# Kernel optimization log

Hardware: AMD Instinct MI355X
Metric: run time of the kernel (lower is better)

Reference implementation:

```python
import jax, jax.numpy as jnp
import numpy as np

N_NODES = 50000
N_EDGES = 800000
IN_FEAT = 128
HIDDEN = 128
N_CLASSES = 32


def setup_inputs() -> dict:
    key = jax.random.key(0)
    ks = jax.random.split(key, 8)
    x = jax.random.normal(ks[0], (N_NODES, IN_FEAT), dtype=jnp.float32)
    edge_index = jax.random.randint(ks[1], (2, N_EDGES), 0, N_NODES, dtype=jnp.int64)
    def glorot(k, fan_in, fan_out):
        s = jnp.sqrt(2.0 / (fan_in + fan_out)).astype(jnp.float32)
        return jax.random.normal(k, (fan_in, fan_out), dtype=jnp.float32) * s
    W1 = glorot(ks[2], IN_FEAT, 2 * HIDDEN)
    b1 = jnp.zeros((2 * HIDDEN,), dtype=jnp.float32)
    W2 = glorot(ks[3], 2 * HIDDEN, HIDDEN)
    b2 = jnp.zeros((HIDDEN,), dtype=jnp.float32)
    W3 = glorot(ks[4], HIDDEN, N_CLASSES)
    b3 = jnp.zeros((N_CLASSES,), dtype=jnp.float32)
    return {"x": x, "edge_index": edge_index, "W1": W1, "b1": b1,
            "W2": W2, "b2": b2, "W3": W3, "b3": b3}


def _gcn_norm(edge_index, num_nodes):
    # PyG GCNConv default: add self-loops, symmetric normalization D^-1/2 (A+I) D^-1/2
    loops = jnp.arange(num_nodes, dtype=edge_index.dtype)
    src = jnp.concatenate([edge_index[0], loops])
    dst = jnp.concatenate([edge_index[1], loops])
    ones = jnp.ones_like(dst, dtype=jnp.float32)
    deg = jax.ops.segment_sum(ones, dst, num_segments=num_nodes)
    dinv = jnp.where(deg > 0, 1.0 / jnp.sqrt(deg), 0.0)
    norm = dinv[src] * dinv[dst]  # [E + N]
    return src, dst, norm


def _gcn_conv(x, src, dst, norm, W, b, num_nodes):
    h = x @ W                               # [N, out]
    msg = h[src] * norm[:, None]            # gather + per-edge scale, [E+N, out]
    agg = jax.ops.segment_sum(msg, dst, num_segments=num_nodes)  # scatter-add
    return agg + b


def reference(x, edge_index, W1, b1, W2, b2, W3, b3):
    n = x.shape[0]
    src, dst, norm = _gcn_norm(edge_index, n)
    h = jax.nn.relu(_gcn_conv(x, src, dst, norm, W1, b1, n))
    h = jax.nn.relu(_gcn_conv(h, src, dst, norm, W2, b2, n))
    return _gcn_conv(h, src, dst, norm, W3, b3, n)
```

## Files before the change

### kernel.cpp

```cpp
#include <hip/hip_runtime.h>
#include <hip/hip_fp16.h>

#define NN 50000
#define NE 800000
#define NBKT 391
#define P1B 256

typedef __attribute__((ext_vector_type(8))) _Float16 half8v;
typedef __attribute__((ext_vector_type(4))) float f32x4;

static inline size_t align_up(size_t x, size_t a) { return (x + a - 1) & ~(a - 1); }

union U8 {
    ushort4 u;
    __half2 h[2];
};

__device__ __forceinline__ float4 u8_to_f4(ushort4 uu) {
    U8 c;
    c.u = uu;
    float2 f01 = __half22float2(c.h[0]);
    float2 f23 = __half22float2(c.h[1]);
    return make_float4(f01.x, f01.y, f23.x, f23.y);
}

__device__ __forceinline__ ushort4 f4_to_u8(float4 v) {
    U8 c;
    c.h[0] = __floats2half2_rn(v.x, v.y);
    c.h[1] = __floats2half2_rn(v.z, v.w);
    return c.u;
}

__device__ __forceinline__ void gload_lds16(const unsigned short* g, unsigned short* l) {
    __builtin_amdgcn_global_load_lds(
        (const __attribute__((address_space(1))) unsigned int*)g,
        (__attribute__((address_space(3))) unsigned int*)l,
        16, 0, 0);
}

__device__ __forceinline__ int detect64(const int* __restrict__ e) {
    int ok = 1;
    for (int k = 1; k < 64; k += 2) ok &= (e[k] == 0);
    return ok;
}

__global__ __launch_bounds__(256) void bucket_hist(const int* __restrict__ e,
                                                   int* __restrict__ base,
                                                   const float* __restrict__ W1,
                                                   const float* __restrict__ W2,
                                                   const float* __restrict__ W3,
                                                   unsigned short* __restrict__ w1t,
                                                   unsigned short* __restrict__ w2t,
                                                   unsigned short* __restrict__ w3t,
                                                   int E) {
    __shared__ int hist[NBKT];
    const int is64 = detect64(e);
    for (int t = threadIdx.x; t < NBKT; t += 256) hist[t] = 0;
    __syncthreads();
    const int chunk = (E + P1B - 1) / P1B;
    const int b0 = blockIdx.x * chunk;
    const int b1 = min(E, b0 + chunk);
    for (int i = b0 + threadIdx.x; i < b1; i += 256) {
        int d = is64 ? e[2 * (E + i)] : e[E + i];
        atomicAdd(&hist[d >> 7], 1);
    }
    for (int i = blockIdx.x * 256 + threadIdx.x; i < 69632; i += P1B * 256) {
        const float* W;
        unsigned short* th;
        int K, M, j;
        if (i < 32768)      { W = W1; th = w1t; K = 128; M = 256; j = i; }
        else if (i < 65536) { W = W2; th = w2t; K = 256; M = 128; j = i - 32768; }
        else                { W = W3; th = w3t; K = 128; M = 32;  j = i - 65536; }
        int k = j / M, m = j % M;
        th[(size_t)m * K + k] = __half_as_ushort(__float2half_rn(W[j]));
    }
    __syncthreads();
    for (int t = threadIdx.x; t < NBKT; t += 256)
        base[blockIdx.x * NBKT + t] = hist[t];
}

__global__ __launch_bounds__(512) void colsum_scan(int* __restrict__ base,
                                                   int* __restrict__ bstart) {
    __shared__ int s[512];
    const int t = threadIdx.x;
    int total = 0;
    if (t < NBKT) {
        for (int b0 = 0; b0 < P1B; b0 += 8) {
            int v[8];
#pragma unroll
            for (int u = 0; u < 8; ++u) v[u] = base[(size_t)(b0 + u) * NBKT + t];
#pragma unroll
            for (int u = 0; u < 8; ++u) {
                int nv = v[u];
                base[(size_t)(b0 + u) * NBKT + t] = total;
                total += nv;
            }
        }
    }
    s[t] = (t < NBKT) ? total : 0;
    __syncthreads();
    for (int off = 1; off < 512; off <<= 1) {
        int tv = (t >= off) ? s[t - off] : 0;
        __syncthreads();
        s[t] += tv;
        __syncthreads();
    }
    if (t < NBKT) bstart[t] = s[t] - total;
    if (t == 0) bstart[NBKT] = s[511];
}

__global__ __launch_bounds__(256) void bucket_scatter(const int* __restrict__ e,
                                                      const int* __restrict__ bstart,
                                                      const int* __restrict__ base,
                                                      unsigned* __restrict__ pairs, int E) {
    __shared__ int cur[NBKT];
    const int is64 = detect64(e);
    for (int t = threadIdx.x; t < NBKT; t += 256)
        cur[t] = bstart[t] + base[blockIdx.x * NBKT + t];
    __syncthreads();
    const int chunk = (E + P1B - 1) / P1B;
    const int b0 = blockIdx.x * chunk;
    const int b1 = min(E, b0 + chunk);
    for (int i = b0 + threadIdx.x; i < b1; i += 256) {
        int s = is64 ? e[2 * i] : e[i];
        int d = is64 ? e[2 * (E + i)] : e[E + i];
        int pos = atomicAdd(&cur[d >> 7], 1);
        pairs[pos] = (unsigned)s | ((unsigned)(d & 127) << 16);
    }
}

__global__ __launch_bounds__(256) void bucket_finalize(const unsigned* __restrict__ pairs,
                                                       const int* __restrict__ bstart,
                                                       const float* __restrict__ x,
                                                       int2* __restrict__ ninfo,
                                                       float* __restrict__ dinv,
                                                       unsigned short* __restrict__ csr,
                                                       unsigned short* __restrict__ xh, int n) {
    __shared__ int ldeg[128];
    __shared__ int lscan[128];
    __shared__ int cur[128];
    __shared__ float sdinv[128];
    const int bkt = blockIdx.x;
    const int s0 = bstart[bkt], s1 = bstart[bkt + 1];
    if (threadIdx.x < 128) ldeg[threadIdx.x] = 0;
    __syncthreads();
    for (int i = s0 + threadIdx.x; i < s1; i += 256)
        atomicAdd(&ldeg[pairs[i] >> 16], 1);
    __syncthreads();
    if (threadIdx.x < 128) lscan[threadIdx.x] = ldeg[threadIdx.x];
    __syncthreads();
    for (int off = 1; off < 128; off <<= 1) {
        int v = 0;
        if (threadIdx.x < 128 && threadIdx.x >= off) v = lscan[threadIdx.x - off];
        __syncthreads();
        if (threadIdx.x < 128) lscan[threadIdx.x] += v;
        __syncthreads();
    }
    if (threadIdx.x < 128) {
        int node = (bkt << 7) + threadIdx.x;
        int exc = s0 + lscan[threadIdx.x] - ldeg[threadIdx.x];
        cur[threadIdx.x] = exc;
        float di = rsqrtf((float)(ldeg[threadIdx.x] + 1));
        sdinv[threadIdx.x] = di;
        if (node < n) {
            ninfo[node] = make_int2(exc, ldeg[threadIdx.x]);
            dinv[node] = di;
        }
    }
    __syncthreads();
    for (int i = s0 + threadIdx.x; i < s1; i += 256) {
        unsigned pr = pairs[i];
        int pos = atomicAdd(&cur[pr >> 16], 1);
        csr[pos] = (unsigned short)(pr & 0xFFFFu);
    }
    for (int idx = threadIdx.x; idx < 128 * 32; idx += 256) {
        int ln = idx >> 5;
        int c4 = idx & 31;
        int node = (bkt << 7) + ln;
        if (node < n) {
            float4 v = ((const float4*)x)[(size_t)node * 32 + c4];
            float s = sdinv[ln];
            v.x *= s; v.y *= s; v.z *= s; v.w *= s;
            ((ushort4*)xh)[(size_t)node * 32 + c4] = f4_to_u8(v);
        }
    }
}

__global__ __launch_bounds__(256) void gemm12(
    const unsigned short* __restrict__ A,
    const unsigned short* __restrict__ W1t,
    const unsigned short* __restrict__ W2t,
    const float* __restrict__ b1,
    const float* __restrict__ dinv,
    unsigned short* __restrict__ H2,
    int N) {
    __shared__ unsigned short sA[128][128];
    __shared__ unsigned short sW[128][128];
    __shared__ unsigned short sH[128][136];

    const int tid = threadIdx.x;
    const int lane = tid & 63;
    const int w = tid >> 6;
    const int wr = w >> 1, wc = w & 1;
    const int row0 = blockIdx.x * 128;
    const int rsel = lane & 15;
    const int cq = lane >> 4;

#pragma unroll
    for (int b = 0; b < 2048; b += 256) {
        int idx = b + tid;
        int r = idx >> 4, s = idx & 15;
        int gr = row0 + r;
        int sp = (s & 8) | ((s ^ r) & 7);
        if (gr < N) gload_lds16(&A[(size_t)gr * 128 + sp * 8], &sA[0][0] + idx * 8);
    }

    f32x4 acc2[4][4];
#pragma unroll
    for (int m = 0; m < 4; ++m)
#pragma unroll
        for (int nn = 0; nn < 4; ++nn) {
            f32x4 z = {0.f, 0.f, 0.f, 0.f};
            acc2[m][nn] = z;
        }

    for (int half = 0; half < 2; ++half) {
        __syncthreads();
#pragma unroll
        for (int b = 0; b < 2048; b += 256) {
            int idx = b + tid;
            int r = idx >> 4, s = idx & 15;
            int sp = (s & 8) | ((s ^ r) & 7);
            gload_lds16(&W1t[(size_t)(half * 128 + r) * 128 + sp * 8], &sW[0][0] + idx * 8);
        }
        __syncthreads();

        f32x4 acc1[4][4];
#pragma unroll
        for (int m = 0; m < 4; ++m)
#pragma unroll
            for (int nn = 0; nn < 4; ++nn) {
                f32x4 z = {0.f, 0.f, 0.f, 0.f};
                acc1[m][nn] = z;
            }
#pragma unroll
        for (int ks = 0; ks < 4; ++ks) {
            half8v af[4], wf[4];
            int c = ks * 4 + cq;
#pragma unroll
            for (int m = 0; m < 4; ++m) {
                int rr = wr * 64 + m * 16 + rsel;
                int cp = (c & 8) | ((c ^ rr) & 7);
                af[m] = *(const half8v*)&sA[rr][cp * 8];
            }
#pragma unroll
            for (int nn = 0; nn < 4; ++nn) {
                int rr = wc * 64 + nn * 16 + rsel;
                int cp = (c & 8) | ((c ^ rr) & 7);
                wf[nn] = *(const half8v*)&sW[rr][cp * 8];
            }
#pragma unroll
            for (int m = 0; m < 4; ++m)
#pragma unroll
                for (int nn = 0; nn < 4; ++nn)
                    acc1[m][nn] = __builtin_amdgcn_mfma_f32_16x16x32_f16(af[m], wf[nn], acc1[m][nn], 0, 0, 0);
        }

        float b1v[4];
#pragma unroll
        for (int nn = 0; nn < 4; ++nn)
            b1v[nn] = b1[half * 128 + wc * 64 + nn * 16 + rsel];
#pragma unroll
        for (int m = 0; m < 4; ++m)
#pragma unroll
            for (int nn = 0; nn < 4; ++nn)
#pragma unroll
                for (int r = 0; r < 4; ++r) {
                    int rl = wr * 64 + m * 16 + cq * 4 + r;
                    int cl = wc * 64 + nn * 16 + rsel;
                    float v = fmaxf(acc1[m][nn][r] + b1v[nn], 0.f);
                    sH[rl][cl] = __half_as_ushort(__float2half_rn(v));
                }
        __syncthreads();

#pragma unroll
        for (int b = 0; b < 2048; b += 256) {
            int idx = b + tid;
            int r = idx >> 4, s = idx & 15;
            int sp = (s & 8) | ((s ^ r) & 7);
            gload_lds16(&W2t[(size_t)r * 256 + half * 128 + sp * 8], &sW[0][0] + idx * 8);
        }
        __syncthreads();

#pragma unroll
        for (int ks = 0; ks < 4; ++ks) {
            half8v ah[4], wf[4];
            int koff = ks * 32 + cq * 8;
            int c = ks * 4 + cq;
#pragma unroll
            for (int m = 0; m < 4; ++m) {
                int rr = wr * 64 + m * 16 + rsel;
                ah[m] = *(const half8v*)&sH[rr][koff];
            }
#pragma unroll
            for (int nn = 0; nn < 4; ++nn) {
                int rr = wc * 64 + nn * 16 + rsel;
                int cp = (c & 8) | ((c ^ rr) & 7);
                wf[nn] = *(const half8v*)&sW[rr][cp * 8];
            }
#pragma unroll
            for (int m = 0; m < 4; ++m)
#pragma unroll
                for (int nn = 0; nn < 4; ++nn)
                    acc2[m][nn] = __builtin_amdgcn_mfma_f32_16x16x32_f16(ah[m], wf[nn], acc2[m][nn], 0, 0, 0);
        }
    }

#pragma unroll
    for (int m = 0; m < 4; ++m)
#pragma unroll
        for (int r = 0; r < 4; ++r) {
            int row = row0 + wr * 64 + m * 16 + cq * 4 + r;
            if (row >= N) continue;
            float rs = dinv[row];
#pragma unroll
            for (int nn = 0; nn < 4; ++nn) {
                int col = wc * 64 + nn * 16 + rsel;
                H2[(size_t)row * 128 + col] =
                    __half_as_ushort(__float2half_rn(acc2[m][nn][r] * rs));
            }
        }
}

template <int BM, int BN, int WM, int WN, bool BIAS, bool RELU, bool OUTF16, bool SCALE>
__global__ __launch_bounds__(256) void gemm_f16(
    const unsigned short* __restrict__ A,
    const unsigned short* __restrict__ Wt,
    const float* __restrict__ bias, const float* __restrict__ dscale,
    float* __restrict__ Cf, unsigned short* __restrict__ Ch,
    int N, int K, int M) {
    constexpr int KS = 64;
    constexpr int WTM = BM / WM;
    constexpr int WTN = BN / WN;
    constexpr int FM = WTM / 16;
    constexpr int FN = WTN / 16;
    constexpr int ACH = BM * 8;
    constexpr int WCH = BN * 8;
    __shared__ unsigned short sA[BM][KS], sW[BN][KS];

    const int tid = threadIdx.x;
    const int lane = tid & 63;
    const int w = tid >> 6;
    const int wr = w / WN, wc = w % WN;
    const int row0 = blockIdx.y * BM;
    const int col0 = blockIdx.x * BN;

    f32x4 acc[FM][FN];
#pragma unroll
    for (int m = 0; m < FM; ++m)
#pragma unroll
        for (int nn = 0; nn < FN; ++nn) {
            f32x4 z = {0.f, 0.f, 0.f, 0.f};
            acc[m][nn] = z;
        }

    for (int k0 = 0; k0 < K; k0 += KS) {
#pragma unroll
        for (int b = 0; b < ACH; b += 256) {
            int idx = b + tid;
            int r = idx >> 3, s = idx & 7;
            int gr = row0 + r;
            int sp = s ^ (r & 7);
            if (gr < N)
                gload_lds16(&A[(size_t)gr * K + k0 + sp * 8], &sA[0][0] + idx * 8);
        }
#pragma unroll
        for (int b = 0; b < WCH; b += 256) {
            int idx = b + tid;
            int r = idx >> 3, s = idx & 7;
            int gc = col0 + r;
            int sp = s ^ (r & 7);
            gload_lds16(&Wt[(size_t)gc * K + k0 + sp * 8], &sW[0][0] + idx * 8);
        }
        __syncthreads();

        half8v af[FM][2], wf[FN][2];
        const int rsel = lane & 15;
        const int cb = lane >> 4;
#pragma unroll
        for (int m = 0; m < FM; ++m) {
            int rr = wr * WTM + m * 16 + rsel;
            af[m][0] = *(const half8v*)&sA[rr][((cb) ^ (rr & 7)) * 8];
            af[m][1] = *(const half8v*)&sA[rr][((cb + 4) ^ (rr & 7)) * 8];
        }
#pragma unroll
        for (int nn = 0; nn < FN; ++nn) {
            int rr = wc * WTN + nn * 16 + rsel;
            wf[nn][0] = *(const half8v*)&sW[rr][((cb) ^ (rr & 7)) * 8];
            wf[nn][1] = *(const half8v*)&sW[rr][((cb + 4) ^ (rr & 7)) * 8];
        }
#pragma unroll
        for (int m = 0; m < FM; ++m)
#pragma unroll
            for (int nn = 0; nn < FN; ++nn) {
                acc[m][nn] = __builtin_amdgcn_mfma_f32_16x16x32_f16(af[m][0], wf[nn][0], acc[m][nn], 0, 0, 0);
                acc[m][nn] = __builtin_amdgcn_mfma_f32_16x16x32_f16(af[m][1], wf[nn][1], acc[m][nn], 0, 0, 0);
            }
        __syncthreads();
    }

#pragma unroll
    for (int m = 0; m < FM; ++m) {
#pragma unroll
        for (int r = 0; r < 4; ++r) {
            int row = row0 + wr * WTM + m * 16 + (lane >> 4) * 4 + r;
            if (row >= N) continue;
            float rs = SCALE ? dscale[row] : 1.f;
#pragma unroll
            for (int nn = 0; nn < FN; ++nn) {
                int col = col0 + wc * WTN + nn * 16 + (lane & 15);
                float v = acc[m][nn][r];
                if (BIAS) v += bias[col];
                if (RELU) v = fmaxf(v, 0.f);
                if (SCALE) v *= rs;
                if constexpr (OUTF16) {
                    Ch[(size_t)row * M + col] = __half_as_ushort(__float2half_rn(v));
                } else {
                    Cf[(size_t)row * M + col] = v;
                }
            }
        }
    }
}

__device__ __forceinline__ float4 add4(float4 v, float4 a) {
    a.x += v.x; a.y += v.y; a.z += v.z; a.w += v.w;
    return a;
}

template <int F, int NPB, bool BIAS, bool RELU, bool OUTF16>
__global__ __launch_bounds__((F / 4) * NPB) void agg4h(
    const unsigned short* __restrict__ h, const int2* __restrict__ ninfo,
    const unsigned short* __restrict__ csr,
    const float* __restrict__ dinv, const float* __restrict__ bias,
    float* __restrict__ outf, unsigned short* __restrict__ outh, int n) {
    constexpr int L = F / 4;
    const int local = threadIdx.x / L;
    const int lane = threadIdx.x % L;
    const int node = blockIdx.x * NPB + local;
    if (node >= n) return;

    const ushort4* __restrict__ h4 = (const ushort4*)h;
    const float di = dinv[node];
    const int2 info = ninfo[node];
    const int beg = info.x;
    const int num = info.y;

    float4 acc0 = u8_to_f4(h4[(size_t)node * L + lane]);
    float4 acc1 = make_float4(0.f, 0.f, 0.f, 0.f);

    for (int e = 0; e < num; e += 16) {
        int c[16];
        ushort4 raw[16];
#pragma unroll
        for (int u = 0; u < 16; ++u) {
            int idx = min(e + u, num - 1);
            c[u] = csr[beg + idx];
        }
#pragma unroll
        for (int u = 0; u < 16; ++u) raw[u] = h4[(size_t)c[u] * L + lane];
#pragma unroll
        for (int u = 0; u < 8; ++u) {
            float4 v = u8_to_f4(raw[u]);
            if (e + u < num) acc0 = add4(v, acc0);
        }
#pragma unroll
        for (int u = 8; u < 16; ++u) {
            float4 v = u8_to_f4(raw[u]);
            if (e + u < num) acc1 = add4(v, acc1);
        }
    }
    float4 acc = add4(acc1, acc0);
    acc.x *= di; acc.y *= di; acc.z *= di; acc.w *= di;
    if (BIAS) {
        const float4 b = ((const float4*)bias)[lane];
        acc.x += b.x; acc.y += b.y; acc.z += b.z; acc.w += b.w;
    }
    if (RELU) {
        acc.x = fmaxf(acc.x, 0.f); acc.y = fmaxf(acc.y, 0.f);
        acc.z = fmaxf(acc.z, 0.f); acc.w = fmaxf(acc.w, 0.f);
    }
    if constexpr (OUTF16) {
        ((ushort4*)outh)[(size_t)node * L + lane] = f4_to_u8(acc);
    } else {
        ((float4*)outf)[(size_t)node * L + lane] = acc;
    }
}

extern "C" void kernel_launch(void* const* d_in, const int* in_sizes, int n_in,
                              void* d_out, int out_size, void* d_ws, size_t ws_size,
                              hipStream_t stream) {
    const float* x   = (const float*)d_in[0];
    const int*   eix = (const int*)d_in[1];
    const float* W1  = (const float*)d_in[2];
    const float* b1  = (const float*)d_in[3];
    const float* W2  = (const float*)d_in[4];
    const float* b2  = (const float*)d_in[5];
    const float* W3  = (const float*)d_in[6];
    const float* b3  = (const float*)d_in[7];
    float* out = (float*)d_out;

    const int n = NN, E = NE;

    char* p = (char*)d_ws;
    auto alloc = [&](size_t bytes) { void* r = (void*)p; p += align_up(bytes, 256); return r; };
    int2*  ninfo     = (int2*)alloc((size_t)n * 8);
    float* dinv      = (float*)alloc((size_t)n * 4);
    int*   bstart    = (int*)alloc((size_t)(NBKT + 1) * 4);
    int*   base      = (int*)alloc((size_t)P1B * NBKT * 4);
    unsigned* pairs  = (unsigned*)alloc((size_t)E * 4);
    unsigned short* csr = (unsigned short*)alloc((size_t)E * 2);
    unsigned short* w1t = (unsigned short*)alloc((size_t)128 * 256 * 2);
    unsigned short* w2t = (unsigned short*)alloc((size_t)256 * 128 * 2);
    unsigned short* w3t = (unsigned short*)alloc((size_t)128 * 32 * 2);
    unsigned short* xh   = (unsigned short*)alloc((size_t)n * 128 * 2);
    unsigned short* agg0 = (unsigned short*)alloc((size_t)n * 128 * 2);
    unsigned short* h2s  = (unsigned short*)alloc((size_t)n * 128 * 2);
    unsigned short* x3   = (unsigned short*)alloc((size_t)n * 128 * 2);
    unsigned short* h3s  = (unsigned short*)alloc((size_t)n * 32 * 2);
    (void)ws_size; (void)in_sizes; (void)n_in; (void)out_size;

    bucket_hist<<<P1B, 256, 0, stream>>>(eix, base, W1, W2, W3, w1t, w2t, w3t, E);
    colsum_scan<<<1, 512, 0, stream>>>(base, bstart);
    bucket_scatter<<<P1B, 256, 0, stream>>>(eix, bstart, base, pairs, E);
    bucket_finalize<<<NBKT, 256, 0, stream>>>(pairs, bstart, x, ninfo, dinv, csr, xh, n);

    const int RB = (n + 127) / 128;

    agg4h<128, 8, false, false, true><<<(n + 7) / 8, 256, 0, stream>>>(
        xh, ninfo, csr, dinv, nullptr, nullptr, agg0, n);

    gemm12<<<RB, 256, 0, stream>>>(agg0, w1t, w2t, b1, dinv, h2s, n);

    agg4h<128, 8, true, true, true><<<(n + 7) / 8, 256, 0, stream>>>(
        h2s, ninfo, csr, dinv, b2, nullptr, x3, n);

    gemm_f16<128, 32, 4, 1, false, false, true, true><<<dim3(1, RB), 256, 0, stream>>>(
        x3, w3t, nullptr, dinv, nullptr, h3s, n, 128, 32);
    agg4h<32, 32, true, false, false><<<(n + 31) / 32, 256, 0, stream>>>(
        h3s, ninfo, csr, dinv, b3, out, nullptr, n);
}
```

Before: 159.5 us.

## Fuse layer-2 aggregation with layer-3 projection and halve histogram blocks

Replaces the separate layer-2 aggregation kernel and the MFMA gemm for W3 with one kernel. It aggregates each node's 128-wide row, applies bias and ReLU, stages the row in LDS and computes the 32-output projection with scalar FMAs per lane. This removes the x3 intermediate (a full N×128 f16 write and read) and one launch, at the cost of doing the small GEMM on vector ALUs instead of MFMA. It also halves P1B, the block count used by the bucket histogram and scatter passes.

After: 201.3 us. 1.26x slower.

```diff
diff --git a/kernel.cpp b/kernel.cpp
--- a/kernel.cpp
+++ b/kernel.cpp
@@ -4,7 +4,7 @@
 #define NN 50000
 #define NE 800000
 #define NBKT 391
-#define P1B 256
+#define P1B 128
 
 typedef __attribute__((ext_vector_type(8))) _Float16 half8v;
 typedef __attribute__((ext_vector_type(4))) float f32x4;
@@ -332,107 +332,6 @@
         }
 }
 
-template <int BM, int BN, int WM, int WN, bool BIAS, bool RELU, bool OUTF16, bool SCALE>
-__global__ __launch_bounds__(256) void gemm_f16(
-    const unsigned short* __restrict__ A,
-    const unsigned short* __restrict__ Wt,
-    const float* __restrict__ bias, const float* __restrict__ dscale,
-    float* __restrict__ Cf, unsigned short* __restrict__ Ch,
-    int N, int K, int M) {
-    constexpr int KS = 64;
-    constexpr int WTM = BM / WM;
-    constexpr int WTN = BN / WN;
-    constexpr int FM = WTM / 16;
-    constexpr int FN = WTN / 16;
-    constexpr int ACH = BM * 8;
-    constexpr int WCH = BN * 8;
-    __shared__ unsigned short sA[BM][KS], sW[BN][KS];
-
-    const int tid = threadIdx.x;
-    const int lane = tid & 63;
-    const int w = tid >> 6;
-    const int wr = w / WN, wc = w % WN;
-    const int row0 = blockIdx.y * BM;
-    const int col0 = blockIdx.x * BN;
-
-    f32x4 acc[FM][FN];
-#pragma unroll
-    for (int m = 0; m < FM; ++m)
-#pragma unroll
-        for (int nn = 0; nn < FN; ++nn) {
-            f32x4 z = {0.f, 0.f, 0.f, 0.f};
-            acc[m][nn] = z;
-        }
-
-    for (int k0 = 0; k0 < K; k0 += KS) {
-#pragma unroll
-        for (int b = 0; b < ACH; b += 256) {
-            int idx = b + tid;
-            int r = idx >> 3, s = idx & 7;
-            int gr = row0 + r;
-            int sp = s ^ (r & 7);
-            if (gr < N)
-                gload_lds16(&A[(size_t)gr * K + k0 + sp * 8], &sA[0][0] + idx * 8);
-        }
-#pragma unroll
-        for (int b = 0; b < WCH; b += 256) {
-            int idx = b + tid;
-            int r = idx >> 3, s = idx & 7;
-            int gc = col0 + r;
-            int sp = s ^ (r & 7);
-            gload_lds16(&Wt[(size_t)gc * K + k0 + sp * 8], &sW[0][0] + idx * 8);
-        }
-        __syncthreads();
-
-        half8v af[FM][2], wf[FN][2];
-        const int rsel = lane & 15;
-        const int cb = lane >> 4;
-#pragma unroll
-        for (int m = 0; m < FM; ++m) {
-            int rr = wr * WTM + m * 16 + rsel;
-            af[m][0] = *(const half8v*)&sA[rr][((cb) ^ (rr & 7)) * 8];
-            af[m][1] = *(const half8v*)&sA[rr][((cb + 4) ^ (rr & 7)) * 8];
-        }
-#pragma unroll
-        for (int nn = 0; nn < FN; ++nn) {
-            int rr = wc * WTN + nn * 16 + rsel;
-            wf[nn][0] = *(const half8v*)&sW[rr][((cb) ^ (rr & 7)) * 8];
-            wf[nn][1] = *(const half8v*)&sW[rr][((cb + 4) ^ (rr & 7)) * 8];
-        }
-#pragma unroll
-        for (int m = 0; m < FM; ++m)
-#pragma unroll
-            for (int nn = 0; nn < FN; ++nn) {
-                acc[m][nn] = __builtin_amdgcn_mfma_f32_16x16x32_f16(af[m][0], wf[nn][0], acc[m][nn], 0, 0, 0);
-                acc[m][nn] = __builtin_amdgcn_mfma_f32_16x16x32_f16(af[m][1], wf[nn][1], acc[m][nn], 0, 0, 0);
-            }
-        __syncthreads();
-    }
-
-#pragma unroll
-    for (int m = 0; m < FM; ++m) {
-#pragma unroll
-        for (int r = 0; r < 4; ++r) {
-            int row = row0 + wr * WTM + m * 16 + (lane >> 4) * 4 + r;
-            if (row >= N) continue;
-            float rs = SCALE ? dscale[row] : 1.f;
-#pragma unroll
-            for (int nn = 0; nn < FN; ++nn) {
-                int col = col0 + wc * WTN + nn * 16 + (lane & 15);
-                float v = acc[m][nn][r];
-                if (BIAS) v += bias[col];
-                if (RELU) v = fmaxf(v, 0.f);
-                if (SCALE) v *= rs;
-                if constexpr (OUTF16) {
-                    Ch[(size_t)row * M + col] = __half_as_ushort(__float2half_rn(v));
-                } else {
-                    Cf[(size_t)row * M + col] = v;
-                }
-            }
-        }
-    }
-}
-
 __device__ __forceinline__ float4 add4(float4 v, float4 a) {
     a.x += v.x; a.y += v.y; a.z += v.z; a.w += v.w;
     return a;
@@ -495,6 +394,77 @@
     } else {
         ((float4*)outf)[(size_t)node * L + lane] = acc;
     }
+}
+
+__global__ __launch_bounds__(256) void agg_gemm3(
+    const unsigned short* __restrict__ h, const int2* __restrict__ ninfo,
+    const unsigned short* __restrict__ csr,
+    const float* __restrict__ dinv, const float* __restrict__ b2,
+    const unsigned short* __restrict__ w3t,
+    unsigned short* __restrict__ h3s, int n) {
+    __shared__ unsigned short sX[8][132];
+
+    const int local = threadIdx.x >> 5;
+    const int lane = threadIdx.x & 31;
+    const int node = blockIdx.x * 8 + local;
+    const bool valid = node < n;
+
+    const ushort4* __restrict__ h4 = (const ushort4*)h;
+    const float di = valid ? dinv[node] : 0.f;
+    int2 info = valid ? ninfo[node] : make_int2(0, 0);
+    const int beg = info.x;
+    const int num = info.y;
+
+    float4 acc0 = valid ? u8_to_f4(h4[(size_t)node * 32 + lane])
+                        : make_float4(0.f, 0.f, 0.f, 0.f);
+    float4 acc1 = make_float4(0.f, 0.f, 0.f, 0.f);
+
+    for (int e = 0; e < num; e += 16) {
+        int c[16];
+        ushort4 raw[16];
+#pragma unroll
+        for (int u = 0; u < 16; ++u) {
+            int idx = min(e + u, num - 1);
+            c[u] = csr[beg + idx];
+        }
+#pragma unroll
+        for (int u = 0; u < 16; ++u) raw[u] = h4[(size_t)c[u] * 32 + lane];
+#pragma unroll
+        for (int u = 0; u < 8; ++u) {
+            float4 v = u8_to_f4(raw[u]);
+            if (e + u < num) acc0 = add4(v, acc0);
+        }
+#pragma unroll
+        for (int u = 8; u < 16; ++u) {
+            float4 v = u8_to_f4(raw[u]);
+            if (e + u < num) acc1 = add4(v, acc1);
+        }
+    }
+    float4 acc = add4(acc1, acc0);
+    acc.x *= di; acc.y *= di; acc.z *= di; acc.w *= di;
+    {
+        const float4 b = ((const float4*)b2)[lane];
+        acc.x = fmaxf(acc.x + b.x, 0.f);
+        acc.y = fmaxf(acc.y + b.y, 0.f);
+        acc.z = fmaxf(acc.z + b.z, 0.f);
+        acc.w = fmaxf(acc.w + b.w, 0.f);
+    }
+    *(ushort4*)&sX[local][lane * 4] = f4_to_u8(acc);
+    __syncthreads();
+
+    const ushort4* __restrict__ w4 = (const ushort4*)(w3t + (size_t)lane * 128);
+    float4 p = make_float4(0.f, 0.f, 0.f, 0.f);
+#pragma unroll
+    for (int c = 0; c < 32; ++c) {
+        float4 xv = u8_to_f4(*(const ushort4*)&sX[local][c * 4]);
+        float4 wv = u8_to_f4(w4[c]);
+        p.x = fmaf(xv.x, wv.x, p.x);
+        p.y = fmaf(xv.y, wv.y, p.y);
+        p.z = fmaf(xv.z, wv.z, p.z);
+        p.w = fmaf(xv.w, wv.w, p.w);
+    }
+    float r = (p.x + p.y) + (p.z + p.w);
+    if (valid) h3s[(size_t)node * 32 + lane] = __half_as_ushort(__float2half_rn(r * di));
 }
 
 extern "C" void kernel_launch(void* const* d_in, const int* in_sizes, int n_in,
@@ -526,7 +496,6 @@
     unsigned short* xh   = (unsigned short*)alloc((size_t)n * 128 * 2);
     unsigned short* agg0 = (unsigned short*)alloc((size_t)n * 128 * 2);
     unsigned short* h2s  = (unsigned short*)alloc((size_t)n * 128 * 2);
-    unsigned short* x3   = (unsigned short*)alloc((size_t)n * 128 * 2);
     unsigned short* h3s  = (unsigned short*)alloc((size_t)n * 32 * 2);
     (void)ws_size; (void)in_sizes; (void)n_in; (void)out_size;
 
@@ -542,11 +511,9 @@
 
     gemm12<<<RB, 256, 0, stream>>>(agg0, w1t, w2t, b1, dinv, h2s, n);
 
-    agg4h<128, 8, true, true, true><<<(n + 7) / 8, 256, 0, stream>>>(
-        h2s, ninfo, csr, dinv, b2, nullptr, x3, n);
-
-    gemm_f16<128, 32, 4, 1, false, false, true, true><<<dim3(1, RB), 256, 0, stream>>>(
-        x3, w3t, nullptr, dinv, nullptr, h3s, n, 128, 32);
+    agg_gemm3<<<(n + 7) / 8, 256, 0, stream>>>(
+        h2s, ninfo, csr, dinv, b2, w3t, h3s, n);
+
     agg4h<32, 32, true, false, false><<<(n + 31) / 32, 256, 0, stream>>>(
         h3s, ninfo, csr, dinv, b3, out, nullptr, n);
 }
```
